# Kernel optimization log

Measured on AMD Instinct MI355X. Metric: run time of the kernel, lower is better.

The kernel has to match this reference:

```python
import jax, jax.numpy as jnp
import numpy as np

B, S, D, H = 2, 2048, 1024, 16
HD = D // H            # head_dim = 64
CHUNK = 1024           # hard-coded in the torch module
ROPE_THETA = 10000.0


def setup_inputs() -> dict:
    key = jax.random.key(0)
    ks = jax.random.split(key, 5)
    hidden_states = jax.random.normal(ks[0], (B, S, D), dtype=jnp.float32)
    # Precomputed RoPE frequencies: freqs_cis[s, j] = exp(i * s * theta_j),
    # stored as real [S, HD//2, 2] = (cos, sin).
    inv_freq = 1.0 / (ROPE_THETA ** (np.arange(0, HD, 2, dtype=np.float32) / HD))
    ang = np.outer(np.arange(S, dtype=np.float32), inv_freq)  # [S, HD//2]
    freqs_cis = jnp.stack([jnp.cos(ang), jnp.sin(ang)], axis=-1).astype(jnp.float32)
    scale = 0.02
    Wq = jax.random.normal(ks[1], (D, D), dtype=jnp.float32) * scale
    Wk = jax.random.normal(ks[2], (D, D), dtype=jnp.float32) * scale
    Wv = jax.random.normal(ks[3], (D, D), dtype=jnp.float32) * scale
    Wo = jax.random.normal(ks[4], (D, D), dtype=jnp.float32) * scale
    return {"hidden_states": hidden_states, "freqs_cis": freqs_cis,
            "Wq": Wq, "Wk": Wk, "Wv": Wv, "Wo": Wo}


def _apply_rope(x, freqs_cis):
    # x: [B, S, H, HD]; freqs_cis: [S, HD//2, 2] (cos, sin)
    b, s, h, hd = x.shape
    xr = x.reshape(b, s, h, hd // 2, 2)
    a, bb = xr[..., 0], xr[..., 1]
    c = freqs_cis[:s, :, 0][None, :, None, :]  # broadcast over batch, heads
    d = freqs_cis[:s, :, 1][None, :, None, :]
    # complex multiply (a + ib)(c + id)
    out = jnp.stack([a * c - bb * d, a * d + bb * c], axis=-1)
    return out.reshape(b, s, h, hd)


def reference(hidden_states, freqs_cis, Wq, Wk, Wv, Wo):
    b, s, dm = hidden_states.shape
    q = (hidden_states @ Wq).reshape(b, s, H, HD)
    k = (hidden_states @ Wk).reshape(b, s, H, HD)
    v = (hidden_states @ Wv).reshape(b, s, H, HD)
    q = _apply_rope(q, freqs_cis)
    k = _apply_rope(k, freqs_cis)
    q = q.transpose(0, 2, 1, 3)  # [B, H, S, HD]
    k = k.transpose(0, 2, 1, 3)
    v = v.transpose(0, 2, 1, 3)
    scaling = HD ** (-0.5)
    out = jnp.zeros_like(q)
    # Faithful replication of the (buggy) chunked attention: softmax is
    # normalized PER key-chunk, then chunk outputs are summed.
    for i in range(0, s, CHUNK):
        j = min(i + CHUNK, s)
        w = jnp.einsum('bhqd,bhkd->bhqk', q, k[:, :, i:j]) * scaling
        w = jax.nn.softmax(w.astype(jnp.float32), axis=-1).astype(q.dtype)
        out = out + jnp.einsum('bhqk,bhkd->bhqd', w, v[:, :, i:j])
    out = out.transpose(0, 2, 1, 3).reshape(b, s, dm)
    return out @ Wo
```

## Files before the change

### kernel.cpp

```cpp
#include <hip/hip_runtime.h>
#include <hip/hip_bf16.h>
#include <cstdint>

typedef __bf16 bf16x8 __attribute__((ext_vector_type(8)));
typedef float f32x4 __attribute__((ext_vector_type(4)));
typedef float f32x16 __attribute__((ext_vector_type(16)));

#define MFMA16(a, b, c) __builtin_amdgcn_mfma_f32_16x16x32_bf16(a, b, c, 0, 0, 0)
#define MFMA32(a, b, c) __builtin_amdgcn_mfma_f32_32x32x16_bf16(a, b, c, 0, 0, 0)

__device__ __forceinline__ void gload_lds16(const void* g, void* l) {
  __builtin_amdgcn_global_load_lds(
      (const __attribute__((address_space(1))) unsigned int*)g,
      (__attribute__((address_space(3))) unsigned int*)l, 16, 0, 0);
}

__device__ __forceinline__ unsigned short f2bf(float x) {
  union { float f; uint32_t u; } v; v.f = x;
  uint32_t r = v.u + 0x7fff + ((v.u >> 16) & 1);
  return (unsigned short)(r >> 16);
}
__device__ __forceinline__ float bf2f(unsigned short h) {
  union { float f; uint32_t u; } v; v.u = ((uint32_t)h) << 16;
  return v.f;
}
__device__ __forceinline__ f32x16 fzero16() {
  f32x16 v;
#pragma unroll
  for (int i = 0; i < 16; ++i) v[i] = 0.f;
  return v;
}

__device__ __forceinline__ void ptrans(const f32x16& sv, float& rsum,
                                       bf16x8& f0, bf16x8& f1) {
  float ps[16];
#pragma unroll
  for (int r = 0; r < 16; ++r) ps[r] = __builtin_exp2f(sv[r]);
  float rs = 0.f;
#pragma unroll
  for (int r = 0; r < 16; ++r) rs += ps[r];
  rsum += rs;
  bf16x8 a, b;
#pragma unroll
  for (int r = 0; r < 8; ++r) a[r] = (__bf16)ps[r];
#pragma unroll
  for (int r = 0; r < 8; ++r) b[r] = (__bf16)ps[8 + r];
  f0 = a; f1 = b;
}

__global__ __launch_bounds__(256) void k_prep(
    const float* __restrict__ hs, const float* __restrict__ Wq,
    const float* __restrict__ Wk, const float* __restrict__ Wv,
    const float* __restrict__ Wo, unsigned short* __restrict__ hsH,
    unsigned short* __restrict__ WtqH, unsigned short* __restrict__ WtkH,
    unsigned short* __restrict__ WtvH, unsigned short* __restrict__ WtoH) {
  __shared__ float tile[32][33];
  const int z = blockIdx.z;
  if (z == 4) {
    int i0 = (blockIdx.y * 32 + blockIdx.x) * 256 + threadIdx.x;
#pragma unroll
    for (int k = 0; k < 4; ++k) {
      int i = i0 + k * 262144;
      float4 v = ((const float4*)hs)[i];
      ushort4 h;
      h.x = f2bf(v.x); h.y = f2bf(v.y); h.z = f2bf(v.z); h.w = f2bf(v.w);
      ((ushort4*)hsH)[i] = h;
    }
    return;
  }
  const float* W = (z == 0) ? Wq : (z == 1) ? Wk : (z == 2) ? Wv : Wo;
  unsigned short* WtH = (z == 0) ? WtqH : (z == 1) ? WtkH : (z == 2) ? WtvH : WtoH;
  const int bx = blockIdx.x, by = blockIdx.y;
  const int tx = threadIdx.x & 31, ty = threadIdx.x >> 5;
#pragma unroll
  for (int i = 0; i < 4; ++i)
    tile[ty + i * 8][tx] = W[(size_t)(by * 32 + ty + i * 8) * 1024 + bx * 32 + tx];
  __syncthreads();
#pragma unroll
  for (int i = 0; i < 4; ++i) {
    float v = tile[tx][ty + i * 8];
    WtH[(size_t)(bx * 32 + ty + i * 8) * 1024 + by * 32 + tx] = f2bf(v);
  }
}

__global__ __launch_bounds__(256, 2) void k_qkv(
    const unsigned short* __restrict__ hsH,
    const unsigned short* __restrict__ WqH, const unsigned short* __restrict__ WkH,
    const unsigned short* __restrict__ WvH, const float* __restrict__ freqs,
    unsigned short* __restrict__ qB, unsigned short* __restrict__ kB,
    unsigned short* __restrict__ vB) {
  __shared__ unsigned short Ah[128 * 32], Bh[128 * 32];
  const int tid = threadIdx.x;
  const int bm = blockIdx.y, bn = blockIdx.x;
  const int w = bn >> 3;
  const int n0 = (bn & 7) * 128;
  const unsigned short* WH = (w == 0) ? WqH : (w == 1) ? WkH : WvH;
  const int lane = tid & 63, wave = tid >> 6;
  const int wm = (wave & 1) * 64, wn = (wave >> 1) * 64;
  const int l15 = lane & 15, lq = lane >> 4;

  f32x4 acc[4][4];
#pragma unroll
  for (int i = 0; i < 4; i++)
#pragma unroll
    for (int j = 0; j < 4; j++) acc[i][j] = (f32x4){0.f, 0.f, 0.f, 0.f};

  const char* baseA = (const char*)hsH + (size_t)(bm * 128) * 2048;
  const char* baseB = (const char*)WH + (size_t)n0 * 2048;
  const int off0 = tid << 4, row0 = off0 >> 6, seg0 = off0 & 63;
  const int off1 = (tid + 256) << 4, row1 = off1 >> 6, seg1 = off1 & 63;

  for (int k0 = 0; k0 < 1024; k0 += 32) {
    __syncthreads();
    gload_lds16(baseA + (size_t)row0 * 2048 + k0 * 2 + seg0, (char*)Ah + wave * 1024);
    gload_lds16(baseB + (size_t)row0 * 2048 + k0 * 2 + seg0, (char*)Bh + wave * 1024);
    gload_lds16(baseA + (size_t)row1 * 2048 + k0 * 2 + seg1,
                (char*)Ah + 4096 + wave * 1024);
    gload_lds16(baseB + (size_t)row1 * 2048 + k0 * 2 + seg1,
                (char*)Bh + 4096 + wave * 1024);
    __syncthreads();
    bf16x8 ah[4], bh[4];
#pragma unroll
    for (int i = 0; i < 4; ++i) {
      ah[i] = *(const bf16x8*)&Ah[(wm + i * 16 + l15) * 32 + lq * 8];
      bh[i] = *(const bf16x8*)&Bh[(wn + i * 16 + l15) * 32 + lq * 8];
    }
#pragma unroll
    for (int i = 0; i < 4; ++i)
#pragma unroll
      for (int j = 0; j < 4; ++j) acc[i][j] = MFMA16(ah[i], bh[j], acc[i][j]);
  }

  unsigned short* dst = (w == 0) ? qB : (w == 1) ? kB : vB;
#pragma unroll
  for (int i = 0; i < 4; ++i) {
#pragma unroll
    for (int j = 0; j < 4; ++j) {
      int colw = n0 + wn + j * 16 + l15;
      int h = colw >> 6, d = colw & 63;
#pragma unroll
      for (int r = 0; r < 4; ++r) {
        int rowg = bm * 128 + wm + i * 16 + lq * 4 + r;
        int s = rowg & 2047, b = rowg >> 11;
        float val = acc[i][j][r];
        size_t bhb = (size_t)(b * 16 + h) * 131072;
        if (w < 2) {
          float partner = __shfl_xor(val, 1);
          int jj = d >> 1;
          float2 cssn = ((const float2*)freqs)[s * 32 + jj];
          float cs = cssn.x, sn = cssn.y;
          float res = (d & 1) ? (partner * sn + val * cs) : (val * cs - partner * sn);
          if (w == 0) {
            res *= 0.18033688011112042f;
            dst[(((size_t)(b * 16 + h)) * 2048 + s) * 64 + d] = f2bf(res);
          } else {
            size_t off = (size_t)(s >> 10) * 65536 + ((s >> 6) & 15) * 4096 +
                         ((s >> 5) & 1) * 2048 + (d >> 4) * 512 +
                         ((s & 31) + 32 * ((d >> 3) & 1)) * 8 + (d & 7);
            dst[bhb + off] = f2bf(res);
          }
        } else {
          int sp = (s & ~12) | ((s & 4) << 1) | ((s & 8) >> 1);
          size_t off = (size_t)(sp >> 10) * 65536 + ((sp >> 6) & 15) * 4096 +
                       (d >> 5) * 2048 + ((sp >> 4) & 3) * 512 +
                       ((d & 31) + 32 * ((sp >> 3) & 1)) * 8 + (sp & 7);
          dst[bhb + off] = f2bf(val);
        }
      }
    }
  }
}

__global__ __launch_bounds__(256, 4) void k_attn(
    const unsigned short* __restrict__ qB, const unsigned short* __restrict__ kB,
    const unsigned short* __restrict__ vB,
    unsigned short* __restrict__ c0, unsigned short* __restrict__ c1) {
  __shared__ unsigned short KV[2][8192];
  const int tid = threadIdx.x, lane = tid & 63, wave = tid >> 6;
  const int l31 = lane & 31, lh = lane >> 5;
  const int bid = blockIdx.x;
  const int x = (bid >> 3) & 15;
  const int gg = (bid & 7) + 8 * (bid >> 7);
  const int bh = gg & 31;
  const int chunk = gg >> 5;
  const int q0 = x * 128 + wave * 32;
  const size_t base = (size_t)bh * 131072;

  bf16x8 qf[4];
#pragma unroll
  for (int ks = 0; ks < 4; ++ks)
    qf[ks] = *(const bf16x8*)(qB + base + (size_t)(q0 + l31) * 64 + ks * 16 + lh * 8);

  const unsigned short* kblk = kB + base + chunk * 65536;
  const unsigned short* vblk = vB + base + chunk * 65536;

  gload_lds16((const char*)kblk + tid * 16, (char*)KV[0] + wave * 1024);
  gload_lds16((const char*)kblk + 4096 + tid * 16, (char*)KV[0] + 4096 + wave * 1024);
  gload_lds16((const char*)vblk + tid * 16, (char*)KV[0] + 8192 + wave * 1024);
  gload_lds16((const char*)vblk + 4096 + tid * 16, (char*)KV[0] + 12288 + wave * 1024);
  __syncthreads();

  f32x16 o[2];
#pragma unroll
  for (int a = 0; a < 2; ++a) o[a] = fzero16();
  float rsum = 0.f;

  for (int kb = 0; kb < 16; ++kb) {
    const unsigned short* Kc = KV[kb & 1];
    const unsigned short* Vc = KV[kb & 1] + 4096;
    if (kb < 15) {
      const char* ks_ = (const char*)(kblk + (kb + 1) * 4096);
      const char* vs_ = (const char*)(vblk + (kb + 1) * 4096);
      char* db = (char*)KV[(kb + 1) & 1];
      gload_lds16(ks_ + tid * 16, db + wave * 1024);
      gload_lds16(ks_ + 4096 + tid * 16, db + 4096 + wave * 1024);
      gload_lds16(vs_ + tid * 16, db + 8192 + wave * 1024);
      gload_lds16(vs_ + 4096 + tid * 16, db + 12288 + wave * 1024);
    }

    f32x16 sA = fzero16(), sB = fzero16();
    {
      bf16x8 kf[4];
#pragma unroll
      for (int ks = 0; ks < 4; ++ks)
        kf[ks] = *(const bf16x8*)(Kc + ks * 512 + lane * 8);
      __builtin_amdgcn_s_setprio(1);
#pragma unroll
      for (int ks = 0; ks < 4; ++ks) sA = MFMA32(kf[ks], qf[ks], sA);
      __builtin_amdgcn_s_setprio(0);
    }
    {
      bf16x8 kf[4];
#pragma unroll
      for (int ks = 0; ks < 4; ++ks)
        kf[ks] = *(const bf16x8*)(Kc + 2048 + ks * 512 + lane * 8);
      __builtin_amdgcn_s_setprio(1);
#pragma unroll
      for (int ks = 0; ks < 4; ++ks) sB = MFMA32(kf[ks], qf[ks], sB);
      __builtin_amdgcn_s_setprio(0);
    }

    bf16x8 vf[2][4];
#pragma unroll
    for (int dt = 0; dt < 2; ++dt)
#pragma unroll
      for (int ks = 0; ks < 4; ++ks)
        vf[dt][ks] = *(const bf16x8*)(Vc + dt * 2048 + ks * 512 + lane * 8);

    bf16x8 fA0, fA1, fB0, fB1;
    ptrans(sA, rsum, fA0, fA1);
    __builtin_amdgcn_s_setprio(1);
    o[0] = MFMA32(vf[0][0], fA0, o[0]);
    o[1] = MFMA32(vf[1][0], fA0, o[1]);
    o[0] = MFMA32(vf[0][1], fA1, o[0]);
    o[1] = MFMA32(vf[1][1], fA1, o[1]);
    __builtin_amdgcn_s_setprio(0);
    ptrans(sB, rsum, fB0, fB1);
    __builtin_amdgcn_s_setprio(1);
    o[0] = MFMA32(vf[0][2], fB0, o[0]);
    o[1] = MFMA32(vf[1][2], fB0, o[1]);
    o[0] = MFMA32(vf[0][3], fB1, o[0]);
    o[1] = MFMA32(vf[1][3], fB1, o[1]);
    __builtin_amdgcn_s_setprio(0);

    __syncthreads();
  }

  unsigned short* cB = chunk ? c1 : c0;
  const int b = bh >> 4, h = bh & 15;
  float lsum = rsum + __shfl_xor(rsum, 32);
  float inv = 1.f / lsum;
  int s = q0 + l31;
#pragma unroll
  for (int dt = 0; dt < 2; ++dt)
#pragma unroll
    for (int g = 0; g < 4; ++g) {
      int d = dt * 32 + 4 * lh + 8 * g;
      size_t idx = ((size_t)(b * 2048 + s)) * 1024 + h * 64 + d;
      ushort4 hv;
#pragma unroll
      for (int t = 0; t < 4; ++t)
        ((unsigned short*)&hv)[t] = f2bf(o[dt][g * 4 + t] * inv);
      *(ushort4*)(cB + idx) = hv;
    }
}

__global__ __launch_bounds__(256) void k_comb(const unsigned short* __restrict__ c0,
                                              const unsigned short* __restrict__ c1,
                                              unsigned short* __restrict__ outB,
                                              int n8) {
  int i = blockIdx.x * blockDim.x + threadIdx.x;
  if (i >= n8) return;
  uint4 a = ((const uint4*)c0)[i];
  uint4 b = ((const uint4*)c1)[i];
  uint4 r;
  const unsigned short* pa = (const unsigned short*)&a;
  const unsigned short* pb = (const unsigned short*)&b;
  unsigned short* pr = (unsigned short*)&r;
#pragma unroll
  for (int j = 0; j < 8; ++j) pr[j] = f2bf(bf2f(pa[j]) + bf2f(pb[j]));
  ((uint4*)outB)[i] = r;
}

__global__ __launch_bounds__(256, 2) void k_out(const unsigned short* __restrict__ A,
                                                const unsigned short* __restrict__ B,
                                                float* __restrict__ out) {
  __shared__ unsigned short Ah[128 * 32], Bh[64 * 32];
  const int tid = threadIdx.x;
  const int bm = blockIdx.y, n0 = blockIdx.x * 64;
  const int lane = tid & 63, wave = tid >> 6;
  const int wm = (wave & 1) * 64, wn = (wave >> 1) * 32;
  const int l15 = lane & 15, lq = lane >> 4;

  f32x4 acc[4][2];
#pragma unroll
  for (int i = 0; i < 4; i++)
#pragma unroll
    for (int j = 0; j < 2; j++) acc[i][j] = (f32x4){0.f, 0.f, 0.f, 0.f};

  const char* baseA = (const char*)A + (size_t)(bm * 128) * 2048;
  const char* baseB = (const char*)B + (size_t)n0 * 2048;
  const int off0 = tid << 4, row0 = off0 >> 6, seg0 = off0 & 63;
  const int off1 = (tid + 256) << 4, row1 = off1 >> 6, seg1 = off1 & 63;

  for (int k0 = 0; k0 < 1024; k0 += 32) {
    __syncthreads();
    gload_lds16(baseA + (size_t)row0 * 2048 + k0 * 2 + seg0, (char*)Ah + wave * 1024);
    gload_lds16(baseA + (size_t)row1 * 2048 + k0 * 2 + seg1,
                (char*)Ah + 4096 + wave * 1024);
    gload_lds16(baseB + (size_t)row0 * 2048 + k0 * 2 + seg0, (char*)Bh + wave * 1024);
    __syncthreads();
    bf16x8 ah[4], bh[2];
#pragma unroll
    for (int i = 0; i < 4; ++i)
      ah[i] = *(const bf16x8*)&Ah[(wm + i * 16 + l15) * 32 + lq * 8];
#pragma unroll
    for (int j = 0; j < 2; ++j)
      bh[j] = *(const bf16x8*)&Bh[(wn + j * 16 + l15) * 32 + lq * 8];
#pragma unroll
    for (int i = 0; i < 4; ++i)
#pragma unroll
      for (int j = 0; j < 2; ++j) acc[i][j] = MFMA16(ah[i], bh[j], acc[i][j]);
  }
#pragma unroll
  for (int i = 0; i < 4; ++i)
#pragma unroll
    for (int j = 0; j < 2; ++j) {
      int colw = n0 + wn + j * 16 + l15;
#pragma unroll
      for (int r = 0; r < 4; ++r) {
        int rowg = bm * 128 + wm + i * 16 + lq * 4 + r;
        out[(size_t)rowg * 1024 + colw] = acc[i][j][r];
      }
    }
}

extern "C" void kernel_launch(void* const* d_in, const int* in_sizes, int n_in,
                              void* d_out, int out_size, void* d_ws, size_t ws_size,
                              hipStream_t stream) {
  const float* hs = (const float*)d_in[0];
  const float* freqs = (const float*)d_in[1];
  const float* Wq = (const float*)d_in[2];
  const float* Wk = (const float*)d_in[3];
  const float* Wv = (const float*)d_in[4];
  const float* Wo = (const float*)d_in[5];
  float* out = (float*)d_out;

  const size_t MD = (size_t)4096 * 1024;
  const size_t WW = (size_t)1024 * 1024;
  unsigned short* hsH = (unsigned short*)d_ws;
  unsigned short* WtqH = hsH + MD;
  unsigned short* WtkH = WtqH + WW;
  unsigned short* WtvH = WtkH + WW;
  unsigned short* WtoH = WtvH + WW;
  unsigned short* qB = WtoH + WW;
  unsigned short* kB = qB + MD;
  unsigned short* vB = kB + MD;
  unsigned short* c0 = vB + MD;
  unsigned short* c1 = c0 + MD;
  unsigned short* attnB = hsH;

  k_prep<<<dim3(32, 32, 5), 256, 0, stream>>>(hs, Wq, Wk, Wv, Wo, hsH,
                                              WtqH, WtkH, WtvH, WtoH);
  k_qkv<<<dim3(24, 32), 256, 0, stream>>>(hsH, WtqH, WtkH, WtvH, freqs, qB, kB, vB);
  k_attn<<<1024, 256, 0, stream>>>(qB, kB, vB, c0, c1);
  k_comb<<<2048, 256, 0, stream>>>(c0, c1, attnB, (int)(MD / 8));
  k_out<<<dim3(16, 32), 256, 0, stream>>>(attnB, WtoH, out);
}
```

Measured before the change: 211.1 us.

## Double-buffer LDS tiles in QKV and output projection GEMMs

Adds two LDS buffers to the QKV and output GEMM kernels. The next K-tile is issued with global_load_lds before the MFMAs on the current tile run, and the loop drops to one barrier per iteration. The goal is to hide global-load latency behind compute. It doubles LDS use per block, which could lower occupancy. The async LDS loads are only ordered by the single barrier, which depends on implicit vmcnt waits at the barrier.

```diff
diff --git a/kernel.cpp b/kernel.cpp
--- a/kernel.cpp
+++ b/kernel.cpp
@@ -89,7 +89,7 @@
     const unsigned short* __restrict__ WvH, const float* __restrict__ freqs,
     unsigned short* __restrict__ qB, unsigned short* __restrict__ kB,
     unsigned short* __restrict__ vB) {
-  __shared__ unsigned short Ah[128 * 32], Bh[128 * 32];
+  __shared__ unsigned short Ah[2][128 * 32], Bh[2][128 * 32];
   const int tid = threadIdx.x;
   const int bm = blockIdx.y, bn = blockIdx.x;
   const int w = bn >> 3;
@@ -110,26 +110,38 @@
   const int off0 = tid << 4, row0 = off0 >> 6, seg0 = off0 & 63;
   const int off1 = (tid + 256) << 4, row1 = off1 >> 6, seg1 = off1 & 63;
 
-  for (int k0 = 0; k0 < 1024; k0 += 32) {
+#define STAGE_QKV(T, BUF)                                                      \
+  {                                                                            \
+    gload_lds16(baseA + (size_t)row0 * 2048 + (T) * 64 + seg0,                 \
+                (char*)Ah[BUF] + wave * 1024);                                 \
+    gload_lds16(baseB + (size_t)row0 * 2048 + (T) * 64 + seg0,                 \
+                (char*)Bh[BUF] + wave * 1024);                                 \
+    gload_lds16(baseA + (size_t)row1 * 2048 + (T) * 64 + seg1,                 \
+                (char*)Ah[BUF] + 4096 + wave * 1024);                          \
+    gload_lds16(baseB + (size_t)row1 * 2048 + (T) * 64 + seg1,                 \
+                (char*)Bh[BUF] + 4096 + wave * 1024);                          \
+  }
+
+  STAGE_QKV(0, 0);
+  __syncthreads();
+
+  for (int t = 0; t < 32; ++t) {
+    if (t < 31) STAGE_QKV(t + 1, (t + 1) & 1);
+    const unsigned short* Ac = Ah[t & 1];
+    const unsigned short* Bc = Bh[t & 1];
+    bf16x8 ah[4], bh[4];
+#pragma unroll
+    for (int i = 0; i < 4; ++i) {
+      ah[i] = *(const bf16x8*)&Ac[(wm + i * 16 + l15) * 32 + lq * 8];
+      bh[i] = *(const bf16x8*)&Bc[(wn + i * 16 + l15) * 32 + lq * 8];
+    }
+#pragma unroll
+    for (int i = 0; i < 4; ++i)
+#pragma unroll
+      for (int j = 0; j < 4; ++j) acc[i][j] = MFMA16(ah[i], bh[j], acc[i][j]);
     __syncthreads();
-    gload_lds16(baseA + (size_t)row0 * 2048 + k0 * 2 + seg0, (char*)Ah + wave * 1024);
-    gload_lds16(baseB + (size_t)row0 * 2048 + k0 * 2 + seg0, (char*)Bh + wave * 1024);
-    gload_lds16(baseA + (size_t)row1 * 2048 + k0 * 2 + seg1,
-                (char*)Ah + 4096 + wave * 1024);
-    gload_lds16(baseB + (size_t)row1 * 2048 + k0 * 2 + seg1,
-                (char*)Bh + 4096 + wave * 1024);
-    __syncthreads();
-    bf16x8 ah[4], bh[4];
-#pragma unroll
-    for (int i = 0; i < 4; ++i) {
-      ah[i] = *(const bf16x8*)&Ah[(wm + i * 16 + l15) * 32 + lq * 8];
-      bh[i] = *(const bf16x8*)&Bh[(wn + i * 16 + l15) * 32 + lq * 8];
-    }
-#pragma unroll
-    for (int i = 0; i < 4; ++i)
-#pragma unroll
-      for (int j = 0; j < 4; ++j) acc[i][j] = MFMA16(ah[i], bh[j], acc[i][j]);
-  }
+  }
+#undef STAGE_QKV
 
   unsigned short* dst = (w == 0) ? qB : (w == 1) ? kB : vB;
 #pragma unroll
@@ -305,7 +317,7 @@
 __global__ __launch_bounds__(256, 2) void k_out(const unsigned short* __restrict__ A,
                                                 const unsigned short* __restrict__ B,
                                                 float* __restrict__ out) {
-  __shared__ unsigned short Ah[128 * 32], Bh[64 * 32];
+  __shared__ unsigned short Ah[2][128 * 32], Bh[2][64 * 32];
   const int tid = threadIdx.x;
   const int bm = blockIdx.y, n0 = blockIdx.x * 64;
   const int lane = tid & 63, wave = tid >> 6;
@@ -323,25 +335,38 @@
   const int off0 = tid << 4, row0 = off0 >> 6, seg0 = off0 & 63;
   const int off1 = (tid + 256) << 4, row1 = off1 >> 6, seg1 = off1 & 63;
 
-  for (int k0 = 0; k0 < 1024; k0 += 32) {
+#define STAGE_OUT(T, BUF)                                                      \
+  {                                                                            \
+    gload_lds16(baseA + (size_t)row0 * 2048 + (T) * 64 + seg0,                 \
+                (char*)Ah[BUF] + wave * 1024);                                 \
+    gload_lds16(baseA + (size_t)row1 * 2048 + (T) * 64 + seg1,                 \
+                (char*)Ah[BUF] + 4096 + wave * 1024);                          \
+    gload_lds16(baseB + (size_t)row0 * 2048 + (T) * 64 + seg0,                 \
+                (char*)Bh[BUF] + wave * 1024);                                 \
+  }
+
+  STAGE_OUT(0, 0);
+  __syncthreads();
+
+  for (int t = 0; t < 32; ++t) {
+    if (t < 31) STAGE_OUT(t + 1, (t + 1) & 1);
+    const unsigned short* Ac = Ah[t & 1];
+    const unsigned short* Bc = Bh[t & 1];
+    bf16x8 ah[4], bh[2];
+#pragma unroll
+    for (int i = 0; i < 4; ++i)
+      ah[i] = *(const bf16x8*)&Ac[(wm + i * 16 + l15) * 32 + lq * 8];
+#pragma unroll
+    for (int j = 0; j < 2; ++j)
+      bh[j] = *(const bf16x8*)&Bc[(wn + j * 16 + l15) * 32 + lq * 8];
+#pragma unroll
+    for (int i = 0; i < 4; ++i)
+#pragma unroll
+      for (int j = 0; j < 2; ++j) acc[i][j] = MFMA16(ah[i], bh[j], acc[i][j]);
     __syncthreads();
-    gload_lds16(baseA + (size_t)row0 * 2048 + k0 * 2 + seg0, (char*)Ah + wave * 1024);
-    gload_lds16(baseA + (size_t)row1 * 2048 + k0 * 2 + seg1,
-                (char*)Ah + 4096 + wave * 1024);
-    gload_lds16(baseB + (size_t)row0 * 2048 + k0 * 2 + seg0, (char*)Bh + wave * 1024);
-    __syncthreads();
-    bf16x8 ah[4], bh[2];
-#pragma unroll
-    for (int i = 0; i < 4; ++i)
-      ah[i] = *(const bf16x8*)&Ah[(wm + i * 16 + l15) * 32 + lq * 8];
-#pragma unroll
-    for (int j = 0; j < 2; ++j)
-      bh[j] = *(const bf16x8*)&Bh[(wn + j * 16 + l15) * 32 + lq * 8];
-#pragma unroll
-    for (int i = 0; i < 4; ++i)
-#pragma unroll
-      for (int j = 0; j < 2; ++j) acc[i][j] = MFMA16(ah[i], bh[j], acc[i][j]);
-  }
+  }
+#undef STAGE_OUT
+
 #pragma unroll
   for (int i = 0; i < 4; ++i)
 #pragma unroll
```

After: 215.9 us. +2.3%, slower.
